# Kernel optimization log

Measured on AMD Instinct MI355X. Metric: run time of the kernel, lower is better.

Reference implementation:

```python
import jax, jax.numpy as jnp
import numpy as np
from jax import lax

A_SCALES = np.array([8., 16., 32.])
A_RATIOS = np.array([0.5, 1., 2.])
STRIDE = 16
PRE_NMS = 6000
POST_NMS = 300
NMS_THRESH = 0.7
MIN_SIZE = 16.0
NEG = -1e9


def _gen_anchors(base_size=16):
    w = h = float(base_size)
    x = y = 0.5 * (base_size - 1)
    size = w * h
    ws = np.round(np.sqrt(size / A_RATIOS))
    hs = np.round(ws * A_RATIOS)
    out = []
    for wi, hi in zip(ws, hs):
        WS = wi * A_SCALES
        HS = hi * A_SCALES
        out.append(np.stack([x - 0.5 * (WS - 1), y - 0.5 * (HS - 1),
                             x + 0.5 * (WS - 1), y + 0.5 * (HS - 1)], 1))
    return np.concatenate(out, 0).astype(np.float32)  # [9,4]

ANCHORS = _gen_anchors()


def _conv(x, w, b, pad):
    y = lax.conv_general_dilated(x, w, (1, 1), [(pad, pad), (pad, pad)],
                                 dimension_numbers=('NCHW', 'OIHW', 'NCHW'))
    return y + b[None, :, None, None]


def _nms(boxes, scores):
    # fixed-size greedy NMS: POST_NMS iterations of argmax + suppress
    areas = (boxes[:, 2] - boxes[:, 0] + 1.) * (boxes[:, 3] - boxes[:, 1] + 1.)
    def step(s, _):
        i = jnp.argmax(s)
        b = boxes[i]
        ix1 = jnp.maximum(b[0], boxes[:, 0]); iy1 = jnp.maximum(b[1], boxes[:, 1])
        ix2 = jnp.minimum(b[2], boxes[:, 2]); iy2 = jnp.minimum(b[3], boxes[:, 3])
        inter = jnp.maximum(ix2 - ix1 + 1., 0.) * jnp.maximum(iy2 - iy1 + 1., 0.)
        iou = inter / (areas[i] + areas - inter)
        return jnp.where(iou > NMS_THRESH, NEG, s), i
    _, keep = lax.scan(step, scores, None, length=POST_NMS)
    return keep


def reference(base_feat, img_info, gt_boxes, W1, b1, Wc, bc, Wb, bb):
    A = ANCHORS.shape[0]  # 9
    h = jax.nn.relu(_conv(base_feat, W1, b1, 1))          # [1,512,H,W]
    scores = _conv(h, Wc, bc, 0)                           # [1,2A,H,W]
    deltas = _conv(h, Wb, bb, 0)                           # [1,4A,H,W]
    H, W = scores.shape[2], scores.shape[3]
    # reshape(2) -> softmax over dim1 -> reshape back (RPN.reshape trick)
    probs = jax.nn.softmax(scores.reshape(1, 2, A * H, W), axis=1).reshape(1, 2 * A, H, W)
    fg = jnp.transpose(probs[0, A:], (1, 2, 0)).reshape(-1)      # [H*W*A], (h,w,a) order
    d = jnp.transpose(deltas[0], (1, 2, 0)).reshape(-1, 4)       # [H*W*A,4]
    sx, sy = jnp.meshgrid(jnp.arange(W, dtype=jnp.float32) * STRIDE,
                          jnp.arange(H, dtype=jnp.float32) * STRIDE)
    shifts = jnp.stack([sx, sy, sx, sy], -1).reshape(-1, 4)      # [H*W,4]
    anch = (shifts[:, None, :] + jnp.asarray(ANCHORS)[None, :, :]).reshape(-1, 4)
    # bbox_transform_inv
    wdt = anch[:, 2] - anch[:, 0] + 1.
    hgt = anch[:, 3] - anch[:, 1] + 1.
    cx = anch[:, 0] + 0.5 * wdt
    cy = anch[:, 1] + 0.5 * hgt
    pcx = d[:, 0] * wdt + cx
    pcy = d[:, 1] * hgt + cy
    pw = jnp.exp(d[:, 2]) * wdt
    ph = jnp.exp(d[:, 3]) * hgt
    x1 = jnp.clip(pcx - 0.5 * pw, 0., img_info[1] - 1.)
    y1 = jnp.clip(pcy - 0.5 * ph, 0., img_info[0] - 1.)
    x2 = jnp.clip(pcx + 0.5 * pw, 0., img_info[1] - 1.)
    y2 = jnp.clip(pcy + 0.5 * ph, 0., img_info[0] - 1.)
    props = jnp.stack([x1, y1, x2, y2], 1)
    ms = MIN_SIZE * img_info[2]
    valid = ((x2 - x1 + 1.) >= ms) & ((y2 - y1 + 1.) >= ms)
    sc = jnp.where(valid, fg, NEG)
    top_sc, top_idx = lax.top_k(sc, PRE_NMS)
    top_boxes = props[top_idx]
    keep = _nms(top_boxes, top_sc)
    out = top_boxes[keep]                                  # [POST_NMS,4]
    return jnp.concatenate([jnp.zeros((POST_NMS, 1), out.dtype), out], 1)


def setup_inputs() -> dict:
    key = jax.random.key(0)
    ks = jax.random.split(key, 6)
    H, W, C = 64, 96, 1024
    base_feat = jax.random.normal(ks[0], (1, C, H, W), jnp.float32)
    img_info = jnp.array([H * 16., W * 16., 1.], jnp.float32)
    gt_boxes = jax.random.uniform(ks[1], (8, 6), jnp.float32) * 100.0
    W1 = jax.random.normal(ks[2], (512, C, 3, 3), jnp.float32) * np.float32(np.sqrt(2.0 / (C * 9)))
    b1 = jnp.zeros((512,), jnp.float32)
    Wc = jax.random.normal(ks[3], (18, 512, 1, 1), jnp.float32) * np.float32(1.0 / np.sqrt(512))
    bc = jnp.zeros((18,), jnp.float32)
    Wb = jax.random.normal(ks[4], (36, 512, 1, 1), jnp.float32) * np.float32(0.01 / np.sqrt(512))
    bb = jnp.zeros((36,), jnp.float32)
    return {"base_feat": base_feat, "img_info": img_info, "gt_boxes": gt_boxes,
            "W1": W1, "b1": b1, "Wc": Wc, "bc": bc, "Wb": Wb, "bb": bb}
```

## Files before the change

kernel.cpp:

```cpp
#include <hip/hip_runtime.h>
#include <math.h>

#define HH 64
#define WW 96
#define NPX (HH*WW)
#define CIN 1024
#define CMID 512
#define NA 9
#define NANCH (NPX*NA)
#define PRE_NMS 6000
#define POST_NMS 300
#define NEGV -1e9f
#define NBINS 16384
#define BUFCAP 8192
#define MASKW 94

#define PYS 66
#define PXS 98
#define NCB 32
#define SCL 2048.0f
#define INV_SCL (1.0f/2048.0f)

#define K2_CS 4
#define K2_CC (CMID/K2_CS)

typedef _Float16 f16x8 __attribute__((ext_vector_type(8)));
typedef float f32x4 __attribute__((ext_vector_type(4)));

__constant__ float c_anch[9][4] = {
    {-84.f, -40.f,  99.f,  55.f},
    {-176.f,-88.f, 191.f, 103.f},
    {-360.f,-184.f,375.f, 199.f},
    {-56.f, -56.f,  71.f,  71.f},
    {-120.f,-120.f,135.f, 135.f},
    {-248.f,-248.f,263.f, 263.f},
    {-36.f, -80.f,  51.f,  95.f},
    {-80.f,-168.f,  95.f, 183.f},
    {-168.f,-344.f,183.f, 359.f}
};

__device__ __forceinline__ unsigned int fkey(float f) {
    unsigned int b = __float_as_uint(f);
    return (b & 0x80000000u) ? ~b : (b | 0x80000000u);
}
__device__ __forceinline__ float fkey_inv(unsigned int k) {
    unsigned int b = (k & 0x80000000u) ? (k & 0x7fffffffu) : ~k;
    return __uint_as_float(b);
}
__device__ __forceinline__ int score_bin(float s) {
    if (!(s > 0.f)) return 0;
    int b = (int)(s * (float)NBINS);
    return b > NBINS - 1 ? NBINS - 1 : b;
}

__global__ __launch_bounds__(256) void prep_all(const float* __restrict__ x,
                                                const float* __restrict__ w,
                                                _Float16* __restrict__ xh,
                                                _Float16* __restrict__ xl,
                                                _Float16* __restrict__ wh,
                                                _Float16* __restrict__ wl) {
    __shared__ char smem[36864];
    int tid = threadIdx.x;
    int bid = blockIdx.x;
    if (bid < 1536) {
        float (*t)[65] = (float(*)[65])smem;
        int c0 = (bid & 15) * 64;
        int p0 = (bid >> 4) * 64;
        int g = tid >> 6, l = tid & 63;
#pragma unroll
        for (int k = 0; k < 16; k++) {
            int cl = g * 16 + k;
            t[cl][l] = x[(size_t)(c0 + cl) * NPX + p0 + l];
        }
        __syncthreads();
#pragma unroll
        for (int k = 0; k < 16; k++) {
            int pl = g * 16 + k;
            int p = p0 + pl;
            int y = p / WW, xc = p - y * WW;
            int c = c0 + l;
            float v = t[l][pl];
            _Float16 hv = (_Float16)v;
            _Float16 lv = (_Float16)((v - (float)hv) * SCL);
            size_t o = (((size_t)(c >> 5) * PYS + (y + 1)) * PXS + (xc + 1)) * 32 + (c & 31);
            xh[o] = hv;
            xl[o] = lv;
        }
    } else {
        _Float16* sh = (_Float16*)smem;
        _Float16* sl = (_Float16*)(smem + 18432);
        int oc = bid - 1536;
        for (int i = tid; i < CIN * 9; i += 256) {
            float v = w[(size_t)oc * CIN * 9 + i];
            _Float16 hv = (_Float16)v;
            sh[i] = hv;
            sl[i] = (_Float16)((v - (float)hv) * SCL);
        }
        __syncthreads();
        for (int i = tid; i < CIN * 9; i += 256) {
            int tap = i >> 10;
            int c = i & 1023;
            size_t o = (((size_t)tap * NCB + (c >> 5)) * CMID + oc) * 32 + (c & 31);
            wh[o] = sh[c * 9 + tap];
            wl[o] = sl[c * 9 + tap];
        }
    }
}

__global__ __launch_bounds__(256, 3) void conv3_mfma(const _Float16* __restrict__ xh,
                                                     const _Float16* __restrict__ xl,
                                                     const _Float16* __restrict__ wh,
                                                     const _Float16* __restrict__ wl,
                                                     const float* __restrict__ b1,
                                                     float* __restrict__ h) {
    __shared__ float4 red[4][2][64];
    int tid = threadIdx.x;
    int lane = tid & 63;
    int wv = tid >> 6;
    int sp = blockIdx.x;
    int ty0 = (sp / 6) * 4;
    int tx0 = (sp % 6) * 16;
    int oc0 = blockIdx.y * 32;

    int la = lane & 15;
    int kg = lane >> 4;

    f32x4 acch[4][2], accc[4][2];
#pragma unroll
    for (int m = 0; m < 4; m++)
#pragma unroll
        for (int n = 0; n < 2; n++) {
            acch[m][n] = (f32x4){0.f, 0.f, 0.f, 0.f};
            accc[m][n] = (f32x4){0.f, 0.f, 0.f, 0.f};
        }

    int cb0 = wv * (NCB / 4);
    for (int cbi = 0; cbi < NCB / 4; cbi++) {
        int cb = cb0 + cbi;
#pragma unroll
        for (int kx = 0; kx < 3; kx++) {
            f16x8 a6h[6], a6l[6];
#pragma unroll
            for (int r = 0; r < 6; r++) {
                int aoff = ((cb * PYS + (ty0 + r)) * PXS + (tx0 + kx + la)) * 32 + kg * 8;
                a6h[r] = *(const f16x8*)(xh + aoff);
                a6l[r] = *(const f16x8*)(xl + aoff);
            }
#pragma unroll
            for (int ky = 0; ky < 3; ky++) {
                const int tap = ky * 3 + kx;
#pragma unroll
                for (int n = 0; n < 2; n++) {
                    int boff = ((tap * NCB + cb) * CMID + oc0 + n * 16 + la) * 32 + kg * 8;
                    f16x8 bh = *(const f16x8*)(wh + boff);
                    f16x8 bl = *(const f16x8*)(wl + boff);
#pragma unroll
                    for (int m = 0; m < 4; m++) {
                        acch[m][n] = __builtin_amdgcn_mfma_f32_16x16x32_f16(a6h[m + ky], bh, acch[m][n], 0, 0, 0);
                        accc[m][n] = __builtin_amdgcn_mfma_f32_16x16x32_f16(a6l[m + ky], bh, accc[m][n], 0, 0, 0);
                        accc[m][n] = __builtin_amdgcn_mfma_f32_16x16x32_f16(a6h[m + ky], bl, accc[m][n], 0, 0, 0);
                    }
                }
            }
        }
    }

#pragma unroll
    for (int m = 0; m < 4; m++) {
        __syncthreads();
#pragma unroll
        for (int n = 0; n < 2; n++) {
            f32x4 t = acch[m][n];
            f32x4 c = accc[m][n];
            float4 w4;
            w4.x = t[0] + c[0] * INV_SCL;
            w4.y = t[1] + c[1] * INV_SCL;
            w4.z = t[2] + c[2] * INV_SCL;
            w4.w = t[3] + c[3] * INV_SCL;
            red[wv][n][lane] = w4;
        }
        __syncthreads();
        if (tid < 128) {
            int n = tid >> 6, l = tid & 63;
            float4 s0 = red[0][n][l], s1 = red[1][n][l];
            float4 s2 = red[2][n][l], s3 = red[3][n][l];
            int oc = oc0 + n * 16 + (l & 15);
            float bs = b1[oc];
            float4 s;
            s.x = fmaxf(s0.x + s1.x + s2.x + s3.x + bs, 0.f);
            s.y = fmaxf(s0.y + s1.y + s2.y + s3.y + bs, 0.f);
            s.z = fmaxf(s0.z + s1.z + s2.z + s3.z + bs, 0.f);
            s.w = fmaxf(s0.w + s1.w + s2.w + s3.w + bs, 0.f);
            int y = ty0 + m;
            int px0 = tx0 + (l >> 4) * 4;
            *(float4*)&h[(size_t)oc * NPX + y * WW + px0] = s;
        }
    }
}

__global__ __launch_bounds__(256) void conv1x1_part(const float* __restrict__ h,
                                                    const float* __restrict__ wc,
                                                    const float* __restrict__ wb,
                                                    float* __restrict__ psum) {
    __shared__ float wT[K2_CC][56];
    int tid = threadIdx.x;
    int px = blockIdx.x * 256 + tid;
    int g = blockIdx.y;
    int cb = g * K2_CC;
    for (int i = tid; i < K2_CC * 54; i += 256) {
        int c = i / 54, o = i - c * 54;
        float wv = (o < 18) ? wc[o * CMID + cb + c] : wb[(o - 18) * CMID + cb + c];
        wT[c][o] = wv;
    }
    __syncthreads();
    float acc[54];
#pragma unroll
    for (int o = 0; o < 54; o++) acc[o] = 0.f;
    for (int c = 0; c < K2_CC; c++) {
        float hv = h[(size_t)(cb + c) * NPX + px];
#pragma unroll
        for (int o = 0; o < 54; o++) acc[o] += wT[c][o] * hv;
    }
    for (int o = 0; o < 54; o++)
        psum[((size_t)g * 54 + o) * NPX + px] = acc[o];
}

__global__ __launch_bounds__(256) void conv1x1_reduce(const float* __restrict__ psum,
                                                      const float* __restrict__ bc,
                                                      const float* __restrict__ bb,
                                                      float* __restrict__ sd) {
    int i = blockIdx.x * 256 + threadIdx.x;
    if (i >= 54 * NPX) return;
    int o = i / NPX;
    float s = (o < 18) ? bc[o] : bb[o - 18];
    for (int g = 0; g < K2_CS; g++) s += psum[(size_t)g * 54 * NPX + i];
    sd[i] = s;
}

__global__ __launch_bounds__(256) void proposals_k(const float* __restrict__ sd,
                                                   const float* __restrict__ info,
                                                   float* __restrict__ props,
                                                   float* __restrict__ scv,
                                                   unsigned int* __restrict__ hist) {
    int i = blockIdx.x * 256 + threadIdx.x;
    if (i >= NANCH) return;
    int a = i % NA;
    int p = i / NA;
    int hy = p / WW, wx = p - hy * WW;

    float s0 = sd[a * NPX + p], s1 = sd[(a + NA) * NPX + p];
    float m = fmaxf(s0, s1);
    float e0 = expf(s0 - m), e1 = expf(s1 - m);
    float fg = e1 / (e0 + e1);

    float d0 = sd[(18 + 4 * a + 0) * NPX + p];
    float d1 = sd[(18 + 4 * a + 1) * NPX + p];
    float d2 = sd[(18 + 4 * a + 2) * NPX + p];
    float d3 = sd[(18 + 4 * a + 3) * NPX + p];

    float sx = wx * 16.f, sy = hy * 16.f;
    float ax1 = c_anch[a][0] + sx, ay1 = c_anch[a][1] + sy;
    float ax2 = c_anch[a][2] + sx, ay2 = c_anch[a][3] + sy;
    float wdt = ax2 - ax1 + 1.f;
    float hgt = ay2 - ay1 + 1.f;
    float cx = ax1 + 0.5f * wdt;
    float cy = ay1 + 0.5f * hgt;
    float pcx = d0 * wdt + cx;
    float pcy = d1 * hgt + cy;
    float pw = expf(d2) * wdt;
    float ph = expf(d3) * hgt;

    float imh = info[0], imw = info[1], iscale = info[2];
    float x1 = fminf(fmaxf(pcx - 0.5f * pw, 0.f), imw - 1.f);
    float y1 = fminf(fmaxf(pcy - 0.5f * ph, 0.f), imh - 1.f);
    float x2 = fminf(fmaxf(pcx + 0.5f * pw, 0.f), imw - 1.f);
    float y2 = fminf(fmaxf(pcy + 0.5f * ph, 0.f), imh - 1.f);

    float ms = 16.f * iscale;
    bool valid = ((x2 - x1 + 1.f) >= ms) && ((y2 - y1 + 1.f) >= ms);
    float s = valid ? fg : NEGV;

    props[(size_t)i * 4 + 0] = x1;
    props[(size_t)i * 4 + 1] = y1;
    props[(size_t)i * 4 + 2] = x2;
    props[(size_t)i * 4 + 3] = y2;
    scv[i] = s;
    atomicAdd(&hist[score_bin(s)], 1u);
}

__global__ __launch_bounds__(1024) void scan_hist(const unsigned int* __restrict__ hist,
                                                  unsigned int* __restrict__ params) {
    __shared__ unsigned int psum[1024];
    int tid = threadIdx.x;
    unsigned int s = 0;
    for (int k = 0; k < 16; k++) s += hist[tid * 16 + k];
    psum[tid] = s;
    __syncthreads();
    if (tid == 0) {
        unsigned int run = 0;
        int B = 0;
        int t;
        for (t = 1023; t >= 0; t--) {
            if (run + psum[t] >= PRE_NMS) break;
            run += psum[t];
        }
        if (t >= 0) {
            unsigned int r2 = run;
            B = t * 16;
            for (int b = t * 16 + 15; b >= t * 16; b--) {
                r2 += hist[b];
                if (r2 >= PRE_NMS) { B = b; break; }
            }
        }
        params[0] = (unsigned int)B;
    }
}

__global__ __launch_bounds__(256) void gather_top(const float* __restrict__ scv,
                                                  const unsigned int* __restrict__ params,
                                                  unsigned long long* __restrict__ buf,
                                                  unsigned int* __restrict__ counter) {
    int i = blockIdx.x * 256 + threadIdx.x;
    if (i >= NANCH) return;
    float s = scv[i];
    if (score_bin(s) >= (int)params[0]) {
        unsigned int pos = atomicAdd(counter, 1u);
        if (pos < BUFCAP) {
            unsigned long long key = ((unsigned long long)fkey(s) << 32) |
                                     (unsigned int)(~(unsigned int)i);
            buf[pos] = key;
        }
    }
}

__global__ __launch_bounds__(1024) void sort_top(unsigned long long* __restrict__ buf,
                                                 const unsigned int* __restrict__ counter,
                                                 const float* __restrict__ props,
                                                 float* __restrict__ top_boxes,
                                                 float* __restrict__ top_sc) {
    __shared__ unsigned long long arr[BUFCAP];
    int tid = threadIdx.x;
    unsigned int m = counter[0];
    if (m > BUFCAP) m = BUFCAP;
    for (int i = tid; i < BUFCAP; i += 1024) arr[i] = (i < (int)m) ? buf[i] : 0ULL;
    __syncthreads();
    for (int k = 2; k <= BUFCAP; k <<= 1) {
        for (int j = k >> 1; j > 0; j >>= 1) {
            for (int i = tid; i < BUFCAP; i += 1024) {
                int l = i ^ j;
                if (l > i) {
                    unsigned long long a = arr[i], b = arr[l];
                    bool dir = ((i & k) == 0);
                    if (dir ? (a < b) : (a > b)) { arr[i] = b; arr[l] = a; }
                }
            }
            __syncthreads();
        }
    }
    for (int t = tid; t < PRE_NMS; t += 1024) {
        unsigned long long v = arr[t];
        unsigned int key = (unsigned int)(v >> 32);
        unsigned int idx = ~((unsigned int)v);
        top_sc[t] = fkey_inv(key);
        float4 bx = *(const float4*)&props[(size_t)idx * 4];
        *(float4*)&top_boxes[(size_t)t * 4] = bx;
    }
}

__global__ __launch_bounds__(256) void iou_mask(const float* __restrict__ top_boxes,
                                                unsigned long long* __restrict__ mask) {
    int wid = (blockIdx.x * 256 + threadIdx.x) >> 6;
    int lane = threadIdx.x & 63;
    if (wid >= PRE_NMS) return;
    float4 b = *(const float4*)&top_boxes[(size_t)wid * 4];
    float ab = (b.z - b.x + 1.f) * (b.w - b.y + 1.f);
    for (int cj = 0; cj < MASKW; cj++) {
        int j = cj * 64 + lane;
        bool sup = false;
        if (j < PRE_NMS) {
            float4 c = *(const float4*)&top_boxes[(size_t)j * 4];
            float ac = (c.z - c.x + 1.f) * (c.w - c.y + 1.f);
            float ix1 = fmaxf(b.x, c.x), iy1 = fmaxf(b.y, c.y);
            float ix2 = fminf(b.z, c.z), iy2 = fminf(b.w, c.w);
            float inter = fmaxf(ix2 - ix1 + 1.f, 0.f) * fmaxf(iy2 - iy1 + 1.f, 0.f);
            float iou = inter / (ab + ac - inter);
            sup = iou > 0.7f;
        }
        unsigned long long m = __ballot(sup);
        if (lane == 0) mask[(size_t)wid * MASKW + cj] = m;
    }
}

__global__ __launch_bounds__(64) void nms_greedy(const float* __restrict__ top_boxes,
                                                 const unsigned long long* __restrict__ mask,
                                                 float* __restrict__ out) {
    int lane = threadIdx.x;
    unsigned long long r0 = 0ULL;
    unsigned long long r1;
    if (lane < 29)      r1 = 0ULL;
    else if (lane == 29) r1 = ~((1ULL << 48) - 1);
    else                r1 = ~0ULL;
    for (int t = 0; t < POST_NMS; t++) {
        unsigned long long w0 = ~r0;
        unsigned long long w1 = ~r1;
        unsigned long long B0 = __ballot(w0 != 0ULL);
        unsigned long long B1 = __ballot(w1 != 0ULL);
        int pos = 0;
        if (B0) {
            int wl = __builtin_ctzll(B0);
            unsigned long long bits = __shfl(w0, wl);
            pos = wl * 64 + __builtin_ctzll(bits);
        } else if (B1) {
            int wl = __builtin_ctzll(B1);
            unsigned long long bits = __shfl(w1, wl);
            pos = (64 + wl) * 64 + __builtin_ctzll(bits);
        }
        if (lane == 0) {
            float4 bb = *(const float4*)&top_boxes[(size_t)pos * 4];
            out[t * 5 + 0] = 0.f;
            out[t * 5 + 1] = bb.x;
            out[t * 5 + 2] = bb.y;
            out[t * 5 + 3] = bb.z;
            out[t * 5 + 4] = bb.w;
        }
        r0 |= mask[(size_t)pos * MASKW + lane];
        if (lane < 30) r1 |= mask[(size_t)pos * MASKW + 64 + lane];
    }
}

extern "C" void kernel_launch(void* const* d_in, const int* in_sizes, int n_in,
                              void* d_out, int out_size, void* d_ws, size_t ws_size,
                              hipStream_t stream) {
    const float* base = (const float*)d_in[0];
    const float* info = (const float*)d_in[1];
    const float* W1 = (const float*)d_in[3];
    const float* b1 = (const float*)d_in[4];
    const float* Wc = (const float*)d_in[5];
    const float* bc = (const float*)d_in[6];
    const float* Wb = (const float*)d_in[7];
    const float* Bb = (const float*)d_in[8];
    float* out = (float*)d_out;
    char* ws = (char*)d_ws;

    const size_t SZ_XT = (size_t)PYS * PXS * CIN * 2;
    const size_t SZ_WT = (size_t)9 * CMID * CIN * 2;
    const size_t OFF_XH = 0;
    const size_t OFF_XL = OFF_XH + SZ_XT;
    const size_t OFF_WH = OFF_XL + SZ_XT;
    const size_t OFF_WL = OFF_WH + SZ_WT;
    const size_t OFF_H  = OFF_WL + SZ_WT;
    const size_t OFF_SD   = OFF_H + (size_t)CMID * NPX * 4;
    const size_t OFF_PROPS= OFF_SD + (size_t)54 * NPX * 4;
    const size_t OFF_SCV  = OFF_PROPS + (size_t)NANCH * 16;
    const size_t OFF_HIST = OFF_SCV + (size_t)NANCH * 4;
    const size_t OFF_PAR  = OFF_HIST + (size_t)NBINS * 4;
    const size_t OFF_BUF  = OFF_PAR + 256;
    const size_t OFF_TB   = OFF_BUF + (size_t)BUFCAP * 8;
    const size_t OFF_TS   = OFF_TB + (size_t)PRE_NMS * 16;
    const size_t OFF_PSUM = OFF_XH;
    const size_t OFF_MASK = OFF_XH;

    _Float16* xh = (_Float16*)(ws + OFF_XH);
    _Float16* xl = (_Float16*)(ws + OFF_XL);
    _Float16* wh = (_Float16*)(ws + OFF_WH);
    _Float16* wl = (_Float16*)(ws + OFF_WL);
    float* h  = (float*)(ws + OFF_H);
    float* psum = (float*)(ws + OFF_PSUM);
    unsigned long long* mask = (unsigned long long*)(ws + OFF_MASK);
    float* sd = (float*)(ws + OFF_SD);
    float* props = (float*)(ws + OFF_PROPS);
    float* scv = (float*)(ws + OFF_SCV);
    unsigned int* hist = (unsigned int*)(ws + OFF_HIST);
    unsigned int* params = (unsigned int*)(ws + OFF_PAR);
    unsigned int* counter = params + 1;
    unsigned long long* buf = (unsigned long long*)(ws + OFF_BUF);
    float* top_boxes = (float*)(ws + OFF_TB);
    float* top_sc = (float*)(ws + OFF_TS);

    hipMemsetAsync(xh, 0, SZ_XT * 2, stream);
    hipMemsetAsync(hist, 0, (size_t)NBINS * 4 + 256, stream);

    prep_all<<<2048, 256, 0, stream>>>(base, W1, xh, xl, wh, wl);
    conv3_mfma<<<dim3(96, 16), 256, 0, stream>>>(xh, xl, wh, wl, b1, h);
    conv1x1_part<<<dim3(NPX / 256, K2_CS), 256, 0, stream>>>(h, Wc, Wb, psum);
    conv1x1_reduce<<<(54 * NPX + 255) / 256, 256, 0, stream>>>(psum, bc, Bb, sd);
    proposals_k<<<NANCH / 256, 256, 0, stream>>>(sd, info, props, scv, hist);
    scan_hist<<<1, 1024, 0, stream>>>(hist, params);
    gather_top<<<NANCH / 256, 256, 0, stream>>>(scv, params, buf, counter);
    sort_top<<<1, 1024, 0, stream>>>(buf, counter, props, top_boxes, top_sc);
    iou_mask<<<(PRE_NMS * 64 + 255) / 256, 256, 0, stream>>>(top_boxes, mask);
    nms_greedy<<<1, 64, 0, stream>>>(top_boxes, mask, out);
}
```

Baseline: 637.0 us.

## Remove split-K reduction in 3x3 conv and skip lower-triangle IoU mask

The 3x3 MFMA conv kernel no longer splits the input channels across the four waves of a block and reduces them through shared memory. Each wave now owns a distinct 4-row spatial tile and loops over all channel blocks for 16 output channels, so the barriers and LDS reduction go away, at the cost of fewer accumulators per wave and less weight reuse across waves. Separately, the IoU mask kernel only computes entries for j >= i and writes zeros below the diagonal, roughly halving the IoU work. This assumes the greedy NMS only reads bits for later-sorted boxes.

Result: slower. 720.2 us (+13.1%).

```diff
diff --git a/kernel.cpp b/kernel.cpp
--- a/kernel.cpp
+++ b/kernel.cpp
@@ -113,30 +113,25 @@
                                                      const _Float16* __restrict__ wl,
                                                      const float* __restrict__ b1,
                                                      float* __restrict__ h) {
-    __shared__ float4 red[4][2][64];
     int tid = threadIdx.x;
     int lane = tid & 63;
     int wv = tid >> 6;
     int sp = blockIdx.x;
-    int ty0 = (sp / 6) * 4;
+    int ty0 = (sp / 6) * 16 + wv * 4;
     int tx0 = (sp % 6) * 16;
-    int oc0 = blockIdx.y * 32;
+    int oc0 = blockIdx.y * 16;
 
     int la = lane & 15;
     int kg = lane >> 4;
 
-    f32x4 acch[4][2], accc[4][2];
-#pragma unroll
-    for (int m = 0; m < 4; m++)
-#pragma unroll
-        for (int n = 0; n < 2; n++) {
-            acch[m][n] = (f32x4){0.f, 0.f, 0.f, 0.f};
-            accc[m][n] = (f32x4){0.f, 0.f, 0.f, 0.f};
-        }
-
-    int cb0 = wv * (NCB / 4);
-    for (int cbi = 0; cbi < NCB / 4; cbi++) {
-        int cb = cb0 + cbi;
+    f32x4 acch[4], accc[4];
+#pragma unroll
+    for (int m = 0; m < 4; m++) {
+        acch[m] = (f32x4){0.f, 0.f, 0.f, 0.f};
+        accc[m] = (f32x4){0.f, 0.f, 0.f, 0.f};
+    }
+
+    for (int cb = 0; cb < NCB; cb++) {
 #pragma unroll
         for (int kx = 0; kx < 3; kx++) {
             f16x8 a6h[6], a6l[6];
@@ -149,52 +144,32 @@
 #pragma unroll
             for (int ky = 0; ky < 3; ky++) {
                 const int tap = ky * 3 + kx;
-#pragma unroll
-                for (int n = 0; n < 2; n++) {
-                    int boff = ((tap * NCB + cb) * CMID + oc0 + n * 16 + la) * 32 + kg * 8;
-                    f16x8 bh = *(const f16x8*)(wh + boff);
-                    f16x8 bl = *(const f16x8*)(wl + boff);
-#pragma unroll
-                    for (int m = 0; m < 4; m++) {
-                        acch[m][n] = __builtin_amdgcn_mfma_f32_16x16x32_f16(a6h[m + ky], bh, acch[m][n], 0, 0, 0);
-                        accc[m][n] = __builtin_amdgcn_mfma_f32_16x16x32_f16(a6l[m + ky], bh, accc[m][n], 0, 0, 0);
-                        accc[m][n] = __builtin_amdgcn_mfma_f32_16x16x32_f16(a6h[m + ky], bl, accc[m][n], 0, 0, 0);
-                    }
+                int boff = ((tap * NCB + cb) * CMID + oc0 + la) * 32 + kg * 8;
+                f16x8 bh = *(const f16x8*)(wh + boff);
+                f16x8 bl = *(const f16x8*)(wl + boff);
+#pragma unroll
+                for (int m = 0; m < 4; m++) {
+                    acch[m] = __builtin_amdgcn_mfma_f32_16x16x32_f16(a6h[m + ky], bh, acch[m], 0, 0, 0);
+                    accc[m] = __builtin_amdgcn_mfma_f32_16x16x32_f16(a6l[m + ky], bh, accc[m], 0, 0, 0);
+                    accc[m] = __builtin_amdgcn_mfma_f32_16x16x32_f16(a6h[m + ky], bl, accc[m], 0, 0, 0);
                 }
             }
         }
     }
 
+    int oc = oc0 + la;
+    float bs = b1[oc];
 #pragma unroll
     for (int m = 0; m < 4; m++) {
-        __syncthreads();
-#pragma unroll
-        for (int n = 0; n < 2; n++) {
-            f32x4 t = acch[m][n];
-            f32x4 c = accc[m][n];
-            float4 w4;
-            w4.x = t[0] + c[0] * INV_SCL;
-            w4.y = t[1] + c[1] * INV_SCL;
-            w4.z = t[2] + c[2] * INV_SCL;
-            w4.w = t[3] + c[3] * INV_SCL;
-            red[wv][n][lane] = w4;
-        }
-        __syncthreads();
-        if (tid < 128) {
-            int n = tid >> 6, l = tid & 63;
-            float4 s0 = red[0][n][l], s1 = red[1][n][l];
-            float4 s2 = red[2][n][l], s3 = red[3][n][l];
-            int oc = oc0 + n * 16 + (l & 15);
-            float bs = b1[oc];
-            float4 s;
-            s.x = fmaxf(s0.x + s1.x + s2.x + s3.x + bs, 0.f);
-            s.y = fmaxf(s0.y + s1.y + s2.y + s3.y + bs, 0.f);
-            s.z = fmaxf(s0.z + s1.z + s2.z + s3.z + bs, 0.f);
-            s.w = fmaxf(s0.w + s1.w + s2.w + s3.w + bs, 0.f);
-            int y = ty0 + m;
-            int px0 = tx0 + (l >> 4) * 4;
-            *(float4*)&h[(size_t)oc * NPX + y * WW + px0] = s;
-        }
+        int y = ty0 + m;
+        f32x4 v = acch[m];
+        f32x4 c = accc[m];
+        float4 o;
+        o.x = fmaxf(v[0] + c[0] * INV_SCL + bs, 0.f);
+        o.y = fmaxf(v[1] + c[1] * INV_SCL + bs, 0.f);
+        o.z = fmaxf(v[2] + c[2] * INV_SCL + bs, 0.f);
+        o.w = fmaxf(v[3] + c[3] * INV_SCL + bs, 0.f);
+        *(float4*)&h[(size_t)oc * NPX + y * WW + tx0 + kg * 4] = o;
     }
 }
 
@@ -375,18 +350,21 @@
     float4 b = *(const float4*)&top_boxes[(size_t)wid * 4];
     float ab = (b.z - b.x + 1.f) * (b.w - b.y + 1.f);
     for (int cj = 0; cj < MASKW; cj++) {
-        int j = cj * 64 + lane;
-        bool sup = false;
-        if (j < PRE_NMS) {
-            float4 c = *(const float4*)&top_boxes[(size_t)j * 4];
-            float ac = (c.z - c.x + 1.f) * (c.w - c.y + 1.f);
-            float ix1 = fmaxf(b.x, c.x), iy1 = fmaxf(b.y, c.y);
-            float ix2 = fminf(b.z, c.z), iy2 = fminf(b.w, c.w);
-            float inter = fmaxf(ix2 - ix1 + 1.f, 0.f) * fmaxf(iy2 - iy1 + 1.f, 0.f);
-            float iou = inter / (ab + ac - inter);
-            sup = iou > 0.7f;
-        }
-        unsigned long long m = __ballot(sup);
+        unsigned long long m = 0ULL;
+        if ((cj + 1) * 64 > wid) {
+            int j = cj * 64 + lane;
+            bool sup = false;
+            if (j < PRE_NMS && j >= wid) {
+                float4 c = *(const float4*)&top_boxes[(size_t)j * 4];
+                float ac = (c.z - c.x + 1.f) * (c.w - c.y + 1.f);
+                float ix1 = fmaxf(b.x, c.x), iy1 = fmaxf(b.y, c.y);
+                float ix2 = fminf(b.z, c.z), iy2 = fminf(b.w, c.w);
+                float inter = fmaxf(ix2 - ix1 + 1.f, 0.f) * fmaxf(iy2 - iy1 + 1.f, 0.f);
+                float iou = inter / (ab + ac - inter);
+                sup = iou > 0.7f;
+            }
+            m = __ballot(sup);
+        }
         if (lane == 0) mask[(size_t)wid * MASKW + cj] = m;
     }
 }
@@ -481,7 +459,7 @@
     hipMemsetAsync(hist, 0, (size_t)NBINS * 4 + 256, stream);
 
     prep_all<<<2048, 256, 0, stream>>>(base, W1, xh, xl, wh, wl);
-    conv3_mfma<<<dim3(96, 16), 256, 0, stream>>>(xh, xl, wh, wl, b1, h);
+    conv3_mfma<<<dim3(24, 32), 256, 0, stream>>>(xh, xl, wh, wl, b1, h);
     conv1x1_part<<<dim3(NPX / 256, K2_CS), 256, 0, stream>>>(h, Wc, Wb, psum);
     conv1x1_reduce<<<(54 * NPX + 255) / 256, 256, 0, stream>>>(psum, bc, Bb, sd);
     proposals_k<<<NANCH / 256, 256, 0, stream>>>(sd, info, props, scv, hist);
```
